# Optimization experiments

Measured on AMD Instinct MI355X. Metric: run time of the kernel, lower is better.

## Reference

```python
import jax, jax.numpy as jnp
import numpy as np

B, S, E, F, N = 2, 1024, 1024, 2048, 8


def setup_inputs() -> dict:
    key = jax.random.key(0)
    k0, k1, k2, k3, k4 = jax.random.split(key, 5)
    x = jax.random.normal(k0, (B, S, E), dtype=jnp.float32)
    # fan_in-scaled params, matching nd_dense_init(1.0, 'fan_in', ...)
    gate_kernel = jax.random.normal(k1, (E, N), dtype=jnp.float32) / np.sqrt(E).astype(np.float32)
    w0 = jax.random.normal(k2, (N, E, F), dtype=jnp.float32) / np.sqrt(E).astype(np.float32)
    w1 = jax.random.normal(k3, (N, E, F), dtype=jnp.float32) / np.sqrt(E).astype(np.float32)
    wo = jax.random.normal(k4, (N, F, E), dtype=jnp.float32) / np.sqrt(F).astype(np.float32)
    return {"x": x, "gate_kernel": gate_kernel, "w0": w0, "w1": w1, "wo": wo, "top_k": 2}


def reference(x, gate_kernel, w0, w1, wo, top_k):
    # x: [B, S, E] -> tokens [T, E]
    b, s, e = x.shape
    n = gate_kernel.shape[-1]
    xf = x.reshape(b * s, e)
    # Router: gate logits + top-k expert selection, softmax over top-k (fp32, as in permute())
    logits = jnp.einsum('te,en->tn', xf, gate_kernel)
    top_w, top_e = jax.lax.top_k(logits, top_k)               # [T, K]
    probs = jax.nn.softmax(top_w.astype(jnp.float32), axis=-1)  # [T, K]
    # Combine weights per (token, expert): scatter top-k probs into [T, N]
    combine = jnp.einsum('tk,tkn->tn', probs, jax.nn.one_hot(top_e, n, dtype=jnp.float32))
    # Expert FFN (dropless): h = silu(x@w0) * (x@w1); out_e = h @ wo   (same math as gmm path)
    h0 = jnp.einsum('te,nef->ntf', xf, w0)                    # [N, T, F]
    h1 = jnp.einsum('te,nef->ntf', xf, w1)
    h = jax.nn.silu(h0) * h1
    expert_out = jnp.einsum('ntf,nfe->nte', h, wo)            # [N, T, E]
    # Weighted combine over experts (matches unpermute's 'BKE,BK->BE' in fp32)
    out = jnp.einsum('nte,tn->te', expert_out, combine)
    return out.reshape(b, s, e)
```

## Files before the change

### kernel.cpp

```cpp
#include <hip/hip_runtime.h>
#include <hip/hip_bf16.h>

#define T_TOK 2048
#define E_DIM 1024
#define F_DIM 2048
#define N_EXP 8

typedef __attribute__((ext_vector_type(8))) short short8;
typedef __attribute__((ext_vector_type(4))) float f32x4;

__device__ __forceinline__ short bf2s(__hip_bfloat16 v) {
  union { __hip_bfloat16 b; short s; } u; u.b = v; return u.s;
}

__device__ __forceinline__ void gload_lds16(const void* g, void* l) {
  __builtin_amdgcn_global_load_lds((const __attribute__((address_space(1))) void*)g,
                                   (__attribute__((address_space(3))) void*)l, 16, 0, 0);
}

__global__ __launch_bounds__(256) void convert_x_kernel(const float* __restrict__ x,
                                                        __hip_bfloat16* __restrict__ xb) {
  size_t i = ((size_t)blockIdx.x * 256 + threadIdx.x) * 8;
  float4 a = *(const float4*)(x + i);
  float4 b = *(const float4*)(x + i + 4);
  short8 o;
  o[0] = bf2s(__float2bfloat16(a.x)); o[1] = bf2s(__float2bfloat16(a.y));
  o[2] = bf2s(__float2bfloat16(a.z)); o[3] = bf2s(__float2bfloat16(a.w));
  o[4] = bf2s(__float2bfloat16(b.x)); o[5] = bf2s(__float2bfloat16(b.y));
  o[6] = bf2s(__float2bfloat16(b.z)); o[7] = bf2s(__float2bfloat16(b.w));
  *(short8*)(xb + i) = o;
}

__global__ __launch_bounds__(256) void transpose_all_kernel(const float* __restrict__ w0,
                                                            const float* __restrict__ w1,
                                                            const float* __restrict__ wo,
                                                            __hip_bfloat16* __restrict__ w0t,
                                                            __hip_bfloat16* __restrict__ w1t,
                                                            __hip_bfloat16* __restrict__ wot) {
  __shared__ float lt[64 * 65];
  int z = blockIdx.z;
  const float* src; __hip_bfloat16* dst;
  int R, C, r0, c0;
  if (z < 16) {
    R = E_DIM; C = F_DIM;
    int e = z & 7;
    src = (z < 8 ? w0 : w1) + (size_t)e * R * C;
    dst = (z < 8 ? w0t : w1t) + (size_t)e * R * C;
    r0 = blockIdx.y * 64; c0 = blockIdx.x * 64;
  } else {
    R = F_DIM; C = E_DIM;
    int e = z - 16;
    src = wo + (size_t)e * R * C;
    dst = wot + (size_t)e * R * C;
    c0 = (blockIdx.x & 15) * 64;
    r0 = (blockIdx.y * 2 + (blockIdx.x >> 4)) * 64;
  }
  int tid = threadIdx.x;
#pragma unroll
  for (int i = 0; i < 4; i++) {
    int chunk = i * 256 + tid;
    int r = chunk >> 4, c4 = (chunk & 15) * 4;
    float4 v = *(const float4*)(src + (size_t)(r0 + r) * C + c0 + c4);
    float* p = &lt[r * 65 + c4];
    p[0] = v.x; p[1] = v.y; p[2] = v.z; p[3] = v.w;
  }
  __syncthreads();
#pragma unroll
  for (int i = 0; i < 2; i++) {
    int chunk = i * 256 + tid;
    int c = chunk >> 3, rr = (chunk & 7) * 8;
    short8 o;
#pragma unroll
    for (int j = 0; j < 8; j++) o[j] = bf2s(__float2bfloat16(lt[(rr + j) * 65 + c]));
    *(short8*)(dst + (size_t)(c0 + c) * R + r0 + rr) = o;
  }
}

__global__ __launch_bounds__(256) void router_kernel(const float* __restrict__ x,
                                                     const float* __restrict__ gk,
                                                     int* __restrict__ tk_e,
                                                     float* __restrict__ tk_p,
                                                     int* __restrict__ counts) {
  int w = threadIdx.x >> 6, l = threadIdx.x & 63;
  int t = blockIdx.x * 4 + w;
  const float* xr = x + (size_t)t * E_DIM;
  double acc[N_EXP];
#pragma unroll
  for (int n = 0; n < N_EXP; n++) acc[n] = 0.0;
  for (int j = 0; j < 16; j++) {
    int i = j * 64 + l;
    double xv = (double)xr[i];
    const float* g = gk + (size_t)i * N_EXP;
#pragma unroll
    for (int n = 0; n < N_EXP; n++) acc[n] += xv * (double)g[n];
  }
#pragma unroll
  for (int off = 32; off > 0; off >>= 1) {
#pragma unroll
    for (int n = 0; n < N_EXP; n++) acc[n] += __shfl_down(acc[n], off);
  }
  if (l == 0) {
    int e1 = 0; double v1 = acc[0];
    for (int n = 1; n < N_EXP; n++) if (acc[n] > v1) { v1 = acc[n]; e1 = n; }
    int e2 = -1; double v2 = -1e300;
    for (int n = 0; n < N_EXP; n++) if (n != e1 && acc[n] > v2) { v2 = acc[n]; e2 = n; }
    float ex = __expf((float)(v2 - v1));
    float p1 = 1.f / (1.f + ex);
    float p2 = ex / (1.f + ex);
    tk_e[t * 2 + 0] = e1; tk_p[t * 2 + 0] = p1;
    tk_e[t * 2 + 1] = e2; tk_p[t * 2 + 1] = p2;
    atomicAdd(&counts[e1], 1);
    atomicAdd(&counts[e2], 1);
  }
}

__global__ __launch_bounds__(256) void scanperm_kernel(const int* __restrict__ tk_e,
                                                       const float* __restrict__ tk_p,
                                                       int* __restrict__ ctrl,
                                                       int* __restrict__ slot_tok,
                                                       float* __restrict__ slot_prob,
                                                       int* __restrict__ inv) {
  __shared__ int offs[8], cur[8];
  int tid = threadIdx.x;
  if (tid == 0) {
    int off = 0, idx = 0;
    for (int e = 0; e < N_EXP; e++) {
      offs[e] = off; cur[e] = 0;
      int c = ctrl[e];
      for (int m0 = 0; m0 < c; m0 += 128) {
        ctrl[32 + idx] = e;
        ctrl[96 + idx] = off + m0;
        ctrl[160 + idx] = (c - m0 < 128) ? (c - m0) : 128;
        idx++;
      }
      off += c;
    }
    ctrl[24] = idx;
  }
  __syncthreads();
  for (int g = tid; g < 2 * T_TOK; g += 256) {
    int e = tk_e[g];
    float p = tk_p[g];
    int pos = atomicAdd(&cur[e], 1);
    int slot = offs[e] + pos;
    slot_tok[slot] = g >> 1;
    slot_prob[slot] = p;
    inv[g] = slot;
  }
}

__global__ __launch_bounds__(512, 4) void gemm1_kernel(const __hip_bfloat16* __restrict__ xb,
                                                       const __hip_bfloat16* __restrict__ w0t,
                                                       const __hip_bfloat16* __restrict__ w1t,
                                                       const int* __restrict__ ctrl,
                                                       const int* __restrict__ slot_tok,
                                                       __hip_bfloat16* __restrict__ h) {
  int lin = blockIdx.x;
  int logical = (lin & 7) * 80 + (lin >> 3);
  int mt = logical % 40;
  int fy = logical / 40;
  if (mt >= ctrl[24]) return;
  int e = ctrl[32 + mt];
  int slot0 = ctrl[96 + mt];
  int rowsv = ctrl[160 + mt];
  int f0 = fy * 128;

  __shared__ alignas(16) short lA[128 * 64];
  __shared__ alignas(16) short lB0[128 * 64];
  __shared__ alignas(16) short lB1[128 * 64];

  int tid = threadIdx.x;
  int w = tid >> 6, l = tid & 63;
  int wm = w >> 2, wn = w & 3;
  int frow = l & 15, fk = l >> 4;

  int r1 = tid >> 3;
  int kc = ((tid & 7) ^ (r1 & 7)) * 8;
  int tokA1 = slot_tok[slot0 + r1];
  int tokA2 = slot_tok[slot0 + r1 + 64];
  const __hip_bfloat16* aS1 = xb + (size_t)tokA1 * E_DIM + kc;
  const __hip_bfloat16* aS2 = xb + (size_t)tokA2 * E_DIM + kc;
  const __hip_bfloat16* b0S1 = w0t + ((size_t)e * F_DIM + f0 + r1) * E_DIM + kc;
  const __hip_bfloat16* b0S2 = b0S1 + (size_t)64 * E_DIM;
  const __hip_bfloat16* b1S1 = w1t + ((size_t)e * F_DIM + f0 + r1) * E_DIM + kc;
  const __hip_bfloat16* b1S2 = b1S1 + (size_t)64 * E_DIM;

  f32x4 zero4 = {0.f, 0.f, 0.f, 0.f};
  f32x4 acc0[4][2], acc1[4][2];
#pragma unroll
  for (int mi = 0; mi < 4; mi++)
#pragma unroll
    for (int ni = 0; ni < 2; ni++) { acc0[mi][ni] = zero4; acc1[mi][ni] = zero4; }

  auto stage = [&](int t) {
    int k0 = t * 64;
    gload_lds16(aS1 + k0,  &lA[w * 512]);
    gload_lds16(aS2 + k0,  &lA[4096 + w * 512]);
    gload_lds16(b0S1 + k0, &lB0[w * 512]);
    gload_lds16(b0S2 + k0, &lB0[4096 + w * 512]);
    gload_lds16(b1S1 + k0, &lB1[w * 512]);
    gload_lds16(b1S2 + k0, &lB1[4096 + w * 512]);
  };

  const int NT = E_DIM / 64;
  for (int t = 0; t < NT; ++t) {
    if (t) __syncthreads();
    stage(t);
    __syncthreads();
    __builtin_amdgcn_s_setprio(1);
#pragma unroll
    for (int ks = 0; ks < 2; ++ks) {
      short8 a[4], b0[2], b1[2];
#pragma unroll
      for (int mi = 0; mi < 4; ++mi) {
        int r = wm * 64 + mi * 16 + frow;
        a[mi] = *(const short8*)&lA[r * 64 + ((ks * 4 + fk) ^ (r & 7)) * 8];
      }
#pragma unroll
      for (int ni = 0; ni < 2; ++ni) {
        int n = wn * 32 + ni * 16 + frow;
        int off = n * 64 + ((ks * 4 + fk) ^ (n & 7)) * 8;
        b0[ni] = *(const short8*)&lB0[off];
        b1[ni] = *(const short8*)&lB1[off];
      }
#pragma unroll
      for (int mi = 0; mi < 4; ++mi)
#pragma unroll
        for (int ni = 0; ni < 2; ++ni) {
          acc0[mi][ni] = __builtin_amdgcn_mfma_f32_16x16x32_bf16(a[mi], b0[ni], acc0[mi][ni], 0, 0, 0);
          acc1[mi][ni] = __builtin_amdgcn_mfma_f32_16x16x32_bf16(a[mi], b1[ni], acc1[mi][ni], 0, 0, 0);
        }
    }
    __builtin_amdgcn_s_setprio(0);
  }

#pragma unroll
  for (int mi = 0; mi < 4; ++mi) {
#pragma unroll
    for (int j = 0; j < 4; ++j) {
      int r = wm * 64 + mi * 16 + fk * 4 + j;
      if (r < rowsv) {
        __hip_bfloat16* hr = h + (size_t)(slot0 + r) * F_DIM + f0 + wn * 32;
#pragma unroll
        for (int ni = 0; ni < 2; ++ni) {
          float v0 = acc0[mi][ni][j];
          float v1 = acc1[mi][ni][j];
          float s = (v0 / (1.f + __expf(-v0))) * v1;
          hr[ni * 16 + frow] = __float2bfloat16(s);
        }
      }
    }
  }
}

__global__ __launch_bounds__(512, 4) void gemm2_kernel(const __hip_bfloat16* __restrict__ h,
                                                       const __hip_bfloat16* __restrict__ wot,
                                                       const int* __restrict__ ctrl,
                                                       const float* __restrict__ slot_prob,
                                                       float* __restrict__ parts) {
  int lin = blockIdx.x;
  int logical = (lin & 7) * 40 + (lin >> 3);
  int mt = logical % 40;
  int ey = logical / 40;
  if (mt >= ctrl[24]) return;
  int e = ctrl[32 + mt];
  int slot0 = ctrl[96 + mt];
  int rowsv = ctrl[160 + mt];
  int e0 = ey * 128;

  __shared__ alignas(16) short lA[128 * 64];
  __shared__ alignas(16) short lB[128 * 64];

  int tid = threadIdx.x;
  int w = tid >> 6, l = tid & 63;
  int wm = w >> 2, wn = w & 3;
  int frow = l & 15, fk = l >> 4;

  int r1 = tid >> 3;
  int kc = ((tid & 7) ^ (r1 & 7)) * 8;
  const __hip_bfloat16* aS1 = h + (size_t)(slot0 + r1) * F_DIM + kc;
  const __hip_bfloat16* aS2 = aS1 + (size_t)64 * F_DIM;
  const __hip_bfloat16* bS1 = wot + ((size_t)e * E_DIM + e0 + r1) * F_DIM + kc;
  const __hip_bfloat16* bS2 = bS1 + (size_t)64 * F_DIM;

  f32x4 zero4 = {0.f, 0.f, 0.f, 0.f};
  f32x4 acc[4][2];
#pragma unroll
  for (int mi = 0; mi < 4; mi++)
#pragma unroll
    for (int ni = 0; ni < 2; ni++) acc[mi][ni] = zero4;

  auto stage = [&](int t) {
    int k0 = t * 64;
    gload_lds16(aS1 + k0, &lA[w * 512]);
    gload_lds16(aS2 + k0, &lA[4096 + w * 512]);
    gload_lds16(bS1 + k0, &lB[w * 512]);
    gload_lds16(bS2 + k0, &lB[4096 + w * 512]);
  };

  const int NT = F_DIM / 64;
  for (int t = 0; t < NT; ++t) {
    if (t) __syncthreads();
    stage(t);
    __syncthreads();
    __builtin_amdgcn_s_setprio(1);
#pragma unroll
    for (int ks = 0; ks < 2; ++ks) {
      short8 a[4], b[2];
#pragma unroll
      for (int mi = 0; mi < 4; ++mi) {
        int r = wm * 64 + mi * 16 + frow;
        a[mi] = *(const short8*)&lA[r * 64 + ((ks * 4 + fk) ^ (r & 7)) * 8];
      }
#pragma unroll
      for (int ni = 0; ni < 2; ++ni) {
        int n = wn * 32 + ni * 16 + frow;
        b[ni] = *(const short8*)&lB[n * 64 + ((ks * 4 + fk) ^ (n & 7)) * 8];
      }
#pragma unroll
      for (int mi = 0; mi < 4; ++mi)
#pragma unroll
        for (int ni = 0; ni < 2; ++ni)
          acc[mi][ni] = __builtin_amdgcn_mfma_f32_16x16x32_bf16(a[mi], b[ni], acc[mi][ni], 0, 0, 0);
    }
    __builtin_amdgcn_s_setprio(0);
  }

#pragma unroll
  for (int mi = 0; mi < 4; ++mi) {
#pragma unroll
    for (int j = 0; j < 4; ++j) {
      int r = wm * 64 + mi * 16 + fk * 4 + j;
      if (r < rowsv) {
        int slot = slot0 + r;
        float p = slot_prob[slot];
        float* pr = parts + (size_t)slot * E_DIM + e0 + wn * 32;
#pragma unroll
        for (int ni = 0; ni < 2; ++ni)
          pr[ni * 16 + frow] = p * acc[mi][ni][j];
      }
    }
  }
}

__global__ __launch_bounds__(256) void combine_kernel(const float* __restrict__ parts,
                                                      const int* __restrict__ inv,
                                                      float* __restrict__ out) {
  int g = blockIdx.x * 256 + threadIdx.x;
  int row = g >> 7, c = (g & 127) * 8;
  int s1 = inv[row * 2], s2 = inv[row * 2 + 1];
  const float4* p1 = (const float4*)(parts + (size_t)s1 * E_DIM + c);
  const float4* p2 = (const float4*)(parts + (size_t)s2 * E_DIM + c);
  float4 a0 = p1[0], a1 = p1[1], b0 = p2[0], b1 = p2[1];
  float4 o0 = {a0.x + b0.x, a0.y + b0.y, a0.z + b0.z, a0.w + b0.w};
  float4 o1 = {a1.x + b1.x, a1.y + b1.y, a1.z + b1.z, a1.w + b1.w};
  float4* op = (float4*)(out + (size_t)row * E_DIM + c);
  op[0] = o0; op[1] = o1;
}

extern "C" void kernel_launch(void* const* d_in, const int* in_sizes, int n_in,
                              void* d_out, int out_size, void* d_ws, size_t ws_size,
                              hipStream_t stream) {
  const float* x  = (const float*)d_in[0];
  const float* gk = (const float*)d_in[1];
  const float* w0 = (const float*)d_in[2];
  const float* w1 = (const float*)d_in[3];
  const float* wo = (const float*)d_in[4];
  float* out = (float*)d_out;
  char* ws = (char*)d_ws;

  const size_t SLOTS = 2 * T_TOK + 128;
  const size_t OFF_XB   = 0;
  const size_t OFF_W0T  = OFF_XB  + (size_t)T_TOK * E_DIM * 2;
  const size_t OFF_W1T  = OFF_W0T + (size_t)N_EXP * E_DIM * F_DIM * 2;
  const size_t OFF_WOT  = OFF_W1T + (size_t)N_EXP * E_DIM * F_DIM * 2;
  const size_t OFF_H    = OFF_WOT + (size_t)N_EXP * F_DIM * E_DIM * 2;
  const size_t OFF_STOK = OFF_H   + SLOTS * F_DIM * 2;
  const size_t OFF_SPRB = OFF_STOK + SLOTS * 4;
  const size_t OFF_TKE  = OFF_SPRB + SLOTS * 4;
  const size_t OFF_TKP  = OFF_TKE + (size_t)2 * T_TOK * 4;
  const size_t OFF_INV  = OFF_TKP + (size_t)2 * T_TOK * 4;
  const size_t OFF_CTRL = OFF_INV + (size_t)2 * T_TOK * 4;
  const size_t NEED     = OFF_CTRL + 1024;
  if (ws_size < NEED) return;

  __hip_bfloat16* xb   = (__hip_bfloat16*)(ws + OFF_XB);
  __hip_bfloat16* w0t  = (__hip_bfloat16*)(ws + OFF_W0T);
  __hip_bfloat16* w1t  = (__hip_bfloat16*)(ws + OFF_W1T);
  __hip_bfloat16* wot  = (__hip_bfloat16*)(ws + OFF_WOT);
  __hip_bfloat16* hbuf = (__hip_bfloat16*)(ws + OFF_H);
  float* parts     = (float*)(ws + OFF_W0T);
  int*   slot_tok  = (int*)(ws + OFF_STOK);
  float* slot_prob = (float*)(ws + OFF_SPRB);
  int*   tk_e      = (int*)(ws + OFF_TKE);
  float* tk_p      = (float*)(ws + OFF_TKP);
  int*   inv       = (int*)(ws + OFF_INV);
  int*   ctrl      = (int*)(ws + OFF_CTRL);

  hipMemsetAsync(ctrl, 0, 1024, stream);
  hipMemsetAsync(slot_tok + 2 * T_TOK, 0, 128 * 4, stream);

  transpose_all_kernel<<<dim3(32, 16, 24), 256, 0, stream>>>(w0, w1, wo, w0t, w1t, wot);
  convert_x_kernel<<<(T_TOK * E_DIM) / (256 * 8), 256, 0, stream>>>(x, xb);
  router_kernel<<<T_TOK / 4, 256, 0, stream>>>(x, gk, tk_e, tk_p, ctrl);
  scanperm_kernel<<<1, 256, 0, stream>>>(tk_e, tk_p, ctrl, slot_tok, slot_prob, inv);
  gemm1_kernel<<<dim3(640), 512, 0, stream>>>(xb, w0t, w1t, ctrl, slot_tok, hbuf);
  gemm2_kernel<<<dim3(320), 512, 0, stream>>>(hbuf, wot, ctrl, slot_prob, parts);
  combine_kernel<<<(T_TOK * 128) / 256, 256, 0, stream>>>(parts, inv, out);
}
```

Baseline: 228.5 us.

## Fuse fp32 weight transpose and bf16 conversion into GEMM B-tile loads

Removes the standalone kernel that transposed and converted all expert weights to bf16. Both GEMM kernels now read fp32 weights directly in their natural layout, convert them to bf16 in registers and write transposed, swizzled short4 chunks into LDS. This avoids a full extra read and write pass over the weights, but every block that shares an expert tile now re-reads fp32 weights (twice the bytes of bf16) and does synchronous register loads instead of async global-to-LDS loads, so load latency is less hidden.

```diff
diff --git a/kernel.cpp b/kernel.cpp
--- a/kernel.cpp
+++ b/kernel.cpp
@@ -8,6 +8,8 @@
 
 typedef __attribute__((ext_vector_type(8))) short short8;
 typedef __attribute__((ext_vector_type(4))) float f32x4;
+
+#define SWZB(f) (((f) ^ ((f) >> 3)) & 7)
 
 __device__ __forceinline__ short bf2s(__hip_bfloat16 v) {
   union { __hip_bfloat16 b; short s; } u; u.b = v; return u.s;
@@ -29,51 +31,6 @@
   o[4] = bf2s(__float2bfloat16(b.x)); o[5] = bf2s(__float2bfloat16(b.y));
   o[6] = bf2s(__float2bfloat16(b.z)); o[7] = bf2s(__float2bfloat16(b.w));
   *(short8*)(xb + i) = o;
-}
-
-__global__ __launch_bounds__(256) void transpose_all_kernel(const float* __restrict__ w0,
-                                                            const float* __restrict__ w1,
-                                                            const float* __restrict__ wo,
-                                                            __hip_bfloat16* __restrict__ w0t,
-                                                            __hip_bfloat16* __restrict__ w1t,
-                                                            __hip_bfloat16* __restrict__ wot) {
-  __shared__ float lt[64 * 65];
-  int z = blockIdx.z;
-  const float* src; __hip_bfloat16* dst;
-  int R, C, r0, c0;
-  if (z < 16) {
-    R = E_DIM; C = F_DIM;
-    int e = z & 7;
-    src = (z < 8 ? w0 : w1) + (size_t)e * R * C;
-    dst = (z < 8 ? w0t : w1t) + (size_t)e * R * C;
-    r0 = blockIdx.y * 64; c0 = blockIdx.x * 64;
-  } else {
-    R = F_DIM; C = E_DIM;
-    int e = z - 16;
-    src = wo + (size_t)e * R * C;
-    dst = wot + (size_t)e * R * C;
-    c0 = (blockIdx.x & 15) * 64;
-    r0 = (blockIdx.y * 2 + (blockIdx.x >> 4)) * 64;
-  }
-  int tid = threadIdx.x;
-#pragma unroll
-  for (int i = 0; i < 4; i++) {
-    int chunk = i * 256 + tid;
-    int r = chunk >> 4, c4 = (chunk & 15) * 4;
-    float4 v = *(const float4*)(src + (size_t)(r0 + r) * C + c0 + c4);
-    float* p = &lt[r * 65 + c4];
-    p[0] = v.x; p[1] = v.y; p[2] = v.z; p[3] = v.w;
-  }
-  __syncthreads();
-#pragma unroll
-  for (int i = 0; i < 2; i++) {
-    int chunk = i * 256 + tid;
-    int c = chunk >> 3, rr = (chunk & 7) * 8;
-    short8 o;
-#pragma unroll
-    for (int j = 0; j < 8; j++) o[j] = bf2s(__float2bfloat16(lt[(rr + j) * 65 + c]));
-    *(short8*)(dst + (size_t)(c0 + c) * R + r0 + rr) = o;
-  }
 }
 
 __global__ __launch_bounds__(256) void router_kernel(const float* __restrict__ x,
@@ -150,8 +107,8 @@
 }
 
 __global__ __launch_bounds__(512, 4) void gemm1_kernel(const __hip_bfloat16* __restrict__ xb,
-                                                       const __hip_bfloat16* __restrict__ w0t,
-                                                       const __hip_bfloat16* __restrict__ w1t,
+                                                       const float* __restrict__ w0,
+                                                       const float* __restrict__ w1,
                                                        const int* __restrict__ ctrl,
                                                        const int* __restrict__ slot_tok,
                                                        __hip_bfloat16* __restrict__ h) {
@@ -175,15 +132,21 @@
   int frow = l & 15, fk = l >> 4;
 
   int r1 = tid >> 3;
-  int kc = ((tid & 7) ^ (r1 & 7)) * 8;
+  int kcA = ((tid & 7) ^ (r1 & 7)) * 8;
   int tokA1 = slot_tok[slot0 + r1];
   int tokA2 = slot_tok[slot0 + r1 + 64];
-  const __hip_bfloat16* aS1 = xb + (size_t)tokA1 * E_DIM + kc;
-  const __hip_bfloat16* aS2 = xb + (size_t)tokA2 * E_DIM + kc;
-  const __hip_bfloat16* b0S1 = w0t + ((size_t)e * F_DIM + f0 + r1) * E_DIM + kc;
-  const __hip_bfloat16* b0S2 = b0S1 + (size_t)64 * E_DIM;
-  const __hip_bfloat16* b1S1 = w1t + ((size_t)e * F_DIM + f0 + r1) * E_DIM + kc;
-  const __hip_bfloat16* b1S2 = b1S1 + (size_t)64 * E_DIM;
+  const __hip_bfloat16* aS1 = xb + (size_t)tokA1 * E_DIM + kcA;
+  const __hip_bfloat16* aS2 = xb + (size_t)tokA2 * E_DIM + kcA;
+
+  int uf = tid & 31, uk = tid >> 5;
+  const float* b0s = w0 + ((size_t)e * E_DIM + uk * 4) * F_DIM + f0 + uf * 4;
+  const float* b1s = w1 + ((size_t)e * E_DIM + uk * 4) * F_DIM + f0 + uf * 4;
+  int elB[4];
+#pragma unroll
+  for (int j = 0; j < 4; ++j) {
+    int f = uf * 4 + j;
+    elB[j] = f * 64 + (((uk >> 1) ^ SWZB(f)) & 7) * 8 + (uk & 1) * 4;
+  }
 
   f32x4 zero4 = {0.f, 0.f, 0.f, 0.f};
   f32x4 acc0[4][2], acc1[4][2];
@@ -191,21 +154,43 @@
   for (int mi = 0; mi < 4; mi++)
 #pragma unroll
     for (int ni = 0; ni < 2; ni++) { acc0[mi][ni] = zero4; acc1[mi][ni] = zero4; }
-
-  auto stage = [&](int t) {
-    int k0 = t * 64;
-    gload_lds16(aS1 + k0,  &lA[w * 512]);
-    gload_lds16(aS2 + k0,  &lA[4096 + w * 512]);
-    gload_lds16(b0S1 + k0, &lB0[w * 512]);
-    gload_lds16(b0S2 + k0, &lB0[4096 + w * 512]);
-    gload_lds16(b1S1 + k0, &lB1[w * 512]);
-    gload_lds16(b1S2 + k0, &lB1[4096 + w * 512]);
-  };
 
   const int NT = E_DIM / 64;
   for (int t = 0; t < NT; ++t) {
     if (t) __syncthreads();
-    stage(t);
+    int k0 = t * 64;
+    gload_lds16(aS1 + k0, &lA[w * 512]);
+    gload_lds16(aS2 + k0, &lA[4096 + w * 512]);
+    {
+      float4 r[4];
+#pragma unroll
+      for (int rr = 0; rr < 4; ++rr)
+        r[rr] = *(const float4*)(b0s + (size_t)(k0 + rr) * F_DIM);
+#pragma unroll
+      for (int j = 0; j < 4; ++j) {
+        short4 q;
+        q.x = bf2s(__float2bfloat16(((const float*)&r[0])[j]));
+        q.y = bf2s(__float2bfloat16(((const float*)&r[1])[j]));
+        q.z = bf2s(__float2bfloat16(((const float*)&r[2])[j]));
+        q.w = bf2s(__float2bfloat16(((const float*)&r[3])[j]));
+        *(short4*)&lB0[elB[j]] = q;
+      }
+    }
+    {
+      float4 r[4];
+#pragma unroll
+      for (int rr = 0; rr < 4; ++rr)
+        r[rr] = *(const float4*)(b1s + (size_t)(k0 + rr) * F_DIM);
+#pragma unroll
+      for (int j = 0; j < 4; ++j) {
+        short4 q;
+        q.x = bf2s(__float2bfloat16(((const float*)&r[0])[j]));
+        q.y = bf2s(__float2bfloat16(((const float*)&r[1])[j]));
+        q.z = bf2s(__float2bfloat16(((const float*)&r[2])[j]));
+        q.w = bf2s(__float2bfloat16(((const float*)&r[3])[j]));
+        *(short4*)&lB1[elB[j]] = q;
+      }
+    }
     __syncthreads();
     __builtin_amdgcn_s_setprio(1);
 #pragma unroll
@@ -219,7 +204,7 @@
 #pragma unroll
       for (int ni = 0; ni < 2; ++ni) {
         int n = wn * 32 + ni * 16 + frow;
-        int off = n * 64 + ((ks * 4 + fk) ^ (n & 7)) * 8;
+        int off = n * 64 + (((ks * 4 + fk) ^ SWZB(n)) & 7) * 8;
         b0[ni] = *(const short8*)&lB0[off];
         b1[ni] = *(const short8*)&lB1[off];
       }
@@ -254,7 +239,7 @@
 }
 
 __global__ __launch_bounds__(512, 4) void gemm2_kernel(const __hip_bfloat16* __restrict__ h,
-                                                       const __hip_bfloat16* __restrict__ wot,
+                                                       const float* __restrict__ wo,
                                                        const int* __restrict__ ctrl,
                                                        const float* __restrict__ slot_prob,
                                                        float* __restrict__ parts) {
@@ -277,11 +262,18 @@
   int frow = l & 15, fk = l >> 4;
 
   int r1 = tid >> 3;
-  int kc = ((tid & 7) ^ (r1 & 7)) * 8;
-  const __hip_bfloat16* aS1 = h + (size_t)(slot0 + r1) * F_DIM + kc;
+  int kcA = ((tid & 7) ^ (r1 & 7)) * 8;
+  const __hip_bfloat16* aS1 = h + (size_t)(slot0 + r1) * F_DIM + kcA;
   const __hip_bfloat16* aS2 = aS1 + (size_t)64 * F_DIM;
-  const __hip_bfloat16* bS1 = wot + ((size_t)e * E_DIM + e0 + r1) * F_DIM + kc;
-  const __hip_bfloat16* bS2 = bS1 + (size_t)64 * F_DIM;
+
+  int ue = tid & 31, uk = tid >> 5;
+  const float* bs = wo + ((size_t)e * F_DIM + uk * 4) * E_DIM + e0 + ue * 4;
+  int elB[4];
+#pragma unroll
+  for (int j = 0; j < 4; ++j) {
+    int f = ue * 4 + j;
+    elB[j] = f * 64 + (((uk >> 1) ^ SWZB(f)) & 7) * 8 + (uk & 1) * 4;
+  }
 
   f32x4 zero4 = {0.f, 0.f, 0.f, 0.f};
   f32x4 acc[4][2];
@@ -290,18 +282,27 @@
 #pragma unroll
     for (int ni = 0; ni < 2; ni++) acc[mi][ni] = zero4;
 
-  auto stage = [&](int t) {
+  const int NT = F_DIM / 64;
+  for (int t = 0; t < NT; ++t) {
+    if (t) __syncthreads();
     int k0 = t * 64;
     gload_lds16(aS1 + k0, &lA[w * 512]);
     gload_lds16(aS2 + k0, &lA[4096 + w * 512]);
-    gload_lds16(bS1 + k0, &lB[w * 512]);
-    gload_lds16(bS2 + k0, &lB[4096 + w * 512]);
-  };
-
-  const int NT = F_DIM / 64;
-  for (int t = 0; t < NT; ++t) {
-    if (t) __syncthreads();
-    stage(t);
+    {
+      float4 r[4];
+#pragma unroll
+      for (int rr = 0; rr < 4; ++rr)
+        r[rr] = *(const float4*)(bs + (size_t)(k0 + rr) * E_DIM);
+#pragma unroll
+      for (int j = 0; j < 4; ++j) {
+        short4 q;
+        q.x = bf2s(__float2bfloat16(((const float*)&r[0])[j]));
+        q.y = bf2s(__float2bfloat16(((const float*)&r[1])[j]));
+        q.z = bf2s(__float2bfloat16(((const float*)&r[2])[j]));
+        q.w = bf2s(__float2bfloat16(((const float*)&r[3])[j]));
+        *(short4*)&lB[elB[j]] = q;
+      }
+    }
     __syncthreads();
     __builtin_amdgcn_s_setprio(1);
 #pragma unroll
@@ -315,7 +316,7 @@
 #pragma unroll
       for (int ni = 0; ni < 2; ++ni) {
         int n = wn * 32 + ni * 16 + frow;
-        b[ni] = *(const short8*)&lB[n * 64 + ((ks * 4 + fk) ^ (n & 7)) * 8];
+        b[ni] = *(const short8*)&lB[n * 64 + (((ks * 4 + fk) ^ SWZB(n)) & 7) * 8];
       }
 #pragma unroll
       for (int mi = 0; mi < 4; ++mi)
@@ -371,11 +372,9 @@
 
   const size_t SLOTS = 2 * T_TOK + 128;
   const size_t OFF_XB   = 0;
-  const size_t OFF_W0T  = OFF_XB  + (size_t)T_TOK * E_DIM * 2;
-  const size_t OFF_W1T  = OFF_W0T + (size_t)N_EXP * E_DIM * F_DIM * 2;
-  const size_t OFF_WOT  = OFF_W1T + (size_t)N_EXP * E_DIM * F_DIM * 2;
-  const size_t OFF_H    = OFF_WOT + (size_t)N_EXP * F_DIM * E_DIM * 2;
-  const size_t OFF_STOK = OFF_H   + SLOTS * F_DIM * 2;
+  const size_t OFF_H    = OFF_XB + (size_t)T_TOK * E_DIM * 2;
+  const size_t OFF_PART = OFF_H + SLOTS * F_DIM * 2;
+  const size_t OFF_STOK = OFF_PART + SLOTS * E_DIM * 4;
   const size_t OFF_SPRB = OFF_STOK + SLOTS * 4;
   const size_t OFF_TKE  = OFF_SPRB + SLOTS * 4;
   const size_t OFF_TKP  = OFF_TKE + (size_t)2 * T_TOK * 4;
@@ -385,11 +384,8 @@
   if (ws_size < NEED) return;
 
   __hip_bfloat16* xb   = (__hip_bfloat16*)(ws + OFF_XB);
-  __hip_bfloat16* w0t  = (__hip_bfloat16*)(ws + OFF_W0T);
-  __hip_bfloat16* w1t  = (__hip_bfloat16*)(ws + OFF_W1T);
-  __hip_bfloat16* wot  = (__hip_bfloat16*)(ws + OFF_WOT);
   __hip_bfloat16* hbuf = (__hip_bfloat16*)(ws + OFF_H);
-  float* parts     = (float*)(ws + OFF_W0T);
+  float* parts     = (float*)(ws + OFF_PART);
   int*   slot_tok  = (int*)(ws + OFF_STOK);
   float* slot_prob = (float*)(ws + OFF_SPRB);
   int*   tk_e      = (int*)(ws + OFF_TKE);
@@ -400,11 +396,10 @@
   hipMemsetAsync(ctrl, 0, 1024, stream);
   hipMemsetAsync(slot_tok + 2 * T_TOK, 0, 128 * 4, stream);
 
-  transpose_all_kernel<<<dim3(32, 16, 24), 256, 0, stream>>>(w0, w1, wo, w0t, w1t, wot);
   convert_x_kernel<<<(T_TOK * E_DIM) / (256 * 8), 256, 0, stream>>>(x, xb);
   router_kernel<<<T_TOK / 4, 256, 0, stream>>>(x, gk, tk_e, tk_p, ctrl);
   scanperm_kernel<<<1, 256, 0, stream>>>(tk_e, tk_p, ctrl, slot_tok, slot_prob, inv);
-  gemm1_kernel<<<dim3(640), 512, 0, stream>>>(xb, w0t, w1t, ctrl, slot_tok, hbuf);
-  gemm2_kernel<<<dim3(320), 512, 0, stream>>>(hbuf, wot, ctrl, slot_prob, parts);
+  gemm1_kernel<<<dim3(640), 512, 0, stream>>>(xb, w0, w1, ctrl, slot_tok, hbuf);
+  gemm2_kernel<<<dim3(320), 512, 0, stream>>>(hbuf, wo, ctrl, slot_prob, parts);
   combine_kernel<<<(T_TOK * 128) / 256, 256, 0, stream>>>(parts, inv, out);
 }
```

After: 221.6 us. -3.0%, faster.

## Double-buffer GEMM LDS tiles with BK=32 and rewrite weight transpose without LDS

Applied to the files above, without the earlier changes.

Both expert GEMM kernels now split LDS into two half-depth (K=32) buffers and prefetch the next tile while MFMAs run on the current one. This cuts the loop from two barriers per iteration to one and lets global-to-LDS loads overlap with compute, using a new XOR swizzle suited to the 32-wide rows. The weight transpose kernel drops shared memory: each thread loads 8 rows of float4 and writes transposed short8 bf16 vectors directly, with out-of-range blocks exiting early. The risks are twice as many loop iterations with smaller MFMA batches per barrier, and less coalesced global stores in the transpose.

```diff
diff --git a/kernel.cpp b/kernel.cpp
--- a/kernel.cpp
+++ b/kernel.cpp
@@ -16,6 +16,10 @@
 __device__ __forceinline__ void gload_lds16(const void* g, void* l) {
   __builtin_amdgcn_global_load_lds((const __attribute__((address_space(1))) void*)g,
                                    (__attribute__((address_space(3))) void*)l, 16, 0, 0);
+}
+
+__device__ __forceinline__ int swz_off(int r, int c8) {
+  return (r >> 1) * 64 + (((((r & 1) << 2) | c8) ^ ((r >> 1) & 7)) * 8);
 }
 
 __global__ __launch_bounds__(256) void convert_x_kernel(const float* __restrict__ x,
@@ -37,42 +41,38 @@
                                                             __hip_bfloat16* __restrict__ w0t,
                                                             __hip_bfloat16* __restrict__ w1t,
                                                             __hip_bfloat16* __restrict__ wot) {
-  __shared__ float lt[64 * 65];
   int z = blockIdx.z;
   const float* src; __hip_bfloat16* dst;
-  int R, C, r0, c0;
+  int R, C;
   if (z < 16) {
     R = E_DIM; C = F_DIM;
+    if (blockIdx.y >= 8) return;
     int e = z & 7;
     src = (z < 8 ? w0 : w1) + (size_t)e * R * C;
     dst = (z < 8 ? w0t : w1t) + (size_t)e * R * C;
-    r0 = blockIdx.y * 64; c0 = blockIdx.x * 64;
   } else {
     R = F_DIM; C = E_DIM;
+    if (blockIdx.x >= 16) return;
     int e = z - 16;
     src = wo + (size_t)e * R * C;
     dst = wot + (size_t)e * R * C;
-    c0 = (blockIdx.x & 15) * 64;
-    r0 = (blockIdx.y * 2 + (blockIdx.x >> 4)) * 64;
-  }
-  int tid = threadIdx.x;
-#pragma unroll
-  for (int i = 0; i < 4; i++) {
-    int chunk = i * 256 + tid;
-    int r = chunk >> 4, c4 = (chunk & 15) * 4;
-    float4 v = *(const float4*)(src + (size_t)(r0 + r) * C + c0 + c4);
-    float* p = &lt[r * 65 + c4];
-    p[0] = v.x; p[1] = v.y; p[2] = v.z; p[3] = v.w;
-  }
-  __syncthreads();
-#pragma unroll
-  for (int i = 0; i < 2; i++) {
-    int chunk = i * 256 + tid;
-    int c = chunk >> 3, rr = (chunk & 7) * 8;
-    short8 o;
-#pragma unroll
-    for (int j = 0; j < 8; j++) o[j] = bf2s(__float2bfloat16(lt[(rr + j) * 65 + c]));
-    *(short8*)(dst + (size_t)(c0 + c) * R + r0 + rr) = o;
+  }
+  int r0 = blockIdx.y * 128, c0 = blockIdx.x * 64;
+  int l = threadIdx.x & 63, w = threadIdx.x >> 6;
+  int r = r0 + 32 * w + 8 * (l >> 4);
+  int c = c0 + 4 * (l & 15);
+
+  float4 v[8];
+#pragma unroll
+  for (int i = 0; i < 8; ++i)
+    v[i] = *(const float4*)(src + (size_t)(r + i) * C + c);
+#pragma unroll
+  for (int j = 0; j < 4; ++j) {
+    short8 q;
+#pragma unroll
+    for (int i = 0; i < 8; ++i)
+      q[i] = bf2s(__float2bfloat16(((const float*)&v[i])[j]));
+    *(short8*)(dst + (size_t)(c + j) * R + r) = q;
   }
 }
 
@@ -165,25 +165,23 @@
   int rowsv = ctrl[160 + mt];
   int f0 = fy * 128;
 
-  __shared__ alignas(16) short lA[128 * 64];
-  __shared__ alignas(16) short lB0[128 * 64];
-  __shared__ alignas(16) short lB1[128 * 64];
+  __shared__ alignas(16) short lA[2][128 * 32];
+  __shared__ alignas(16) short lB0[2][128 * 32];
+  __shared__ alignas(16) short lB1[2][128 * 32];
 
   int tid = threadIdx.x;
   int w = tid >> 6, l = tid & 63;
   int wm = w >> 2, wn = w & 3;
   int frow = l & 15, fk = l >> 4;
 
-  int r1 = tid >> 3;
-  int kc = ((tid & 7) ^ (r1 & 7)) * 8;
-  int tokA1 = slot_tok[slot0 + r1];
-  int tokA2 = slot_tok[slot0 + r1 + 64];
-  const __hip_bfloat16* aS1 = xb + (size_t)tokA1 * E_DIM + kc;
-  const __hip_bfloat16* aS2 = xb + (size_t)tokA2 * E_DIM + kc;
-  const __hip_bfloat16* b0S1 = w0t + ((size_t)e * F_DIM + f0 + r1) * E_DIM + kc;
-  const __hip_bfloat16* b0S2 = b0S1 + (size_t)64 * E_DIM;
-  const __hip_bfloat16* b1S1 = w1t + ((size_t)e * F_DIM + f0 + r1) * E_DIM + kc;
-  const __hip_bfloat16* b1S2 = b1S1 + (size_t)64 * E_DIM;
+  int stripe = tid >> 3, pos = tid & 7;
+  int px = pos ^ (stripe & 7);
+  int sr = (stripe << 1) | (px >> 2);
+  int sc = px & 3;
+  int tokA = slot_tok[slot0 + sr];
+  const __hip_bfloat16* aS  = xb + (size_t)tokA * E_DIM + sc * 8;
+  const __hip_bfloat16* b0S = w0t + ((size_t)e * F_DIM + f0 + sr) * E_DIM + sc * 8;
+  const __hip_bfloat16* b1S = w1t + ((size_t)e * F_DIM + f0 + sr) * E_DIM + sc * 8;
 
   f32x4 zero4 = {0.f, 0.f, 0.f, 0.f};
   f32x4 acc0[4][2], acc1[4][2];
@@ -192,46 +190,43 @@
 #pragma unroll
     for (int ni = 0; ni < 2; ni++) { acc0[mi][ni] = zero4; acc1[mi][ni] = zero4; }
 
-  auto stage = [&](int t) {
-    int k0 = t * 64;
-    gload_lds16(aS1 + k0,  &lA[w * 512]);
-    gload_lds16(aS2 + k0,  &lA[4096 + w * 512]);
-    gload_lds16(b0S1 + k0, &lB0[w * 512]);
-    gload_lds16(b0S2 + k0, &lB0[4096 + w * 512]);
-    gload_lds16(b1S1 + k0, &lB1[w * 512]);
-    gload_lds16(b1S2 + k0, &lB1[4096 + w * 512]);
+  auto stage = [&](int t, int buf) {
+    int k0 = t * 32;
+    gload_lds16(aS + k0,  &lA[buf][w * 512]);
+    gload_lds16(b0S + k0, &lB0[buf][w * 512]);
+    gload_lds16(b1S + k0, &lB1[buf][w * 512]);
   };
 
-  const int NT = E_DIM / 64;
+  stage(0, 0);
+  __syncthreads();
+
+  const int NT = E_DIM / 32;
   for (int t = 0; t < NT; ++t) {
-    if (t) __syncthreads();
-    stage(t);
+    int cur = t & 1;
+    if (t + 1 < NT) stage(t + 1, cur ^ 1);
+    __builtin_amdgcn_s_setprio(1);
+    short8 a[4], b0[2], b1[2];
+#pragma unroll
+    for (int mi = 0; mi < 4; ++mi) {
+      int r = wm * 64 + mi * 16 + frow;
+      a[mi] = *(const short8*)&lA[cur][swz_off(r, fk)];
+    }
+#pragma unroll
+    for (int ni = 0; ni < 2; ++ni) {
+      int n = wn * 32 + ni * 16 + frow;
+      int off = swz_off(n, fk);
+      b0[ni] = *(const short8*)&lB0[cur][off];
+      b1[ni] = *(const short8*)&lB1[cur][off];
+    }
+#pragma unroll
+    for (int mi = 0; mi < 4; ++mi)
+#pragma unroll
+      for (int ni = 0; ni < 2; ++ni) {
+        acc0[mi][ni] = __builtin_amdgcn_mfma_f32_16x16x32_bf16(a[mi], b0[ni], acc0[mi][ni], 0, 0, 0);
+        acc1[mi][ni] = __builtin_amdgcn_mfma_f32_16x16x32_bf16(a[mi], b1[ni], acc1[mi][ni], 0, 0, 0);
+      }
+    __builtin_amdgcn_s_setprio(0);
     __syncthreads();
-    __builtin_amdgcn_s_setprio(1);
-#pragma unroll
-    for (int ks = 0; ks < 2; ++ks) {
-      short8 a[4], b0[2], b1[2];
-#pragma unroll
-      for (int mi = 0; mi < 4; ++mi) {
-        int r = wm * 64 + mi * 16 + frow;
-        a[mi] = *(const short8*)&lA[r * 64 + ((ks * 4 + fk) ^ (r & 7)) * 8];
-      }
-#pragma unroll
-      for (int ni = 0; ni < 2; ++ni) {
-        int n = wn * 32 + ni * 16 + frow;
-        int off = n * 64 + ((ks * 4 + fk) ^ (n & 7)) * 8;
-        b0[ni] = *(const short8*)&lB0[off];
-        b1[ni] = *(const short8*)&lB1[off];
-      }
-#pragma unroll
-      for (int mi = 0; mi < 4; ++mi)
-#pragma unroll
-        for (int ni = 0; ni < 2; ++ni) {
-          acc0[mi][ni] = __builtin_amdgcn_mfma_f32_16x16x32_bf16(a[mi], b0[ni], acc0[mi][ni], 0, 0, 0);
-          acc1[mi][ni] = __builtin_amdgcn_mfma_f32_16x16x32_bf16(a[mi], b1[ni], acc1[mi][ni], 0, 0, 0);
-        }
-    }
-    __builtin_amdgcn_s_setprio(0);
   }
 
 #pragma unroll
@@ -268,20 +263,20 @@
   int rowsv = ctrl[160 + mt];
   int e0 = ey * 128;
 
-  __shared__ alignas(16) short lA[128 * 64];
-  __shared__ alignas(16) short lB[128 * 64];
+  __shared__ alignas(16) short lA[2][128 * 32];
+  __shared__ alignas(16) short lB[2][128 * 32];
 
   int tid = threadIdx.x;
   int w = tid >> 6, l = tid & 63;
   int wm = w >> 2, wn = w & 3;
   int frow = l & 15, fk = l >> 4;
 
-  int r1 = tid >> 3;
-  int kc = ((tid & 7) ^ (r1 & 7)) * 8;
-  const __hip_bfloat16* aS1 = h + (size_t)(slot0 + r1) * F_DIM + kc;
-  const __hip_bfloat16* aS2 = aS1 + (size_t)64 * F_DIM;
-  const __hip_bfloat16* bS1 = wot + ((size_t)e * E_DIM + e0 + r1) * F_DIM + kc;
-  const __hip_bfloat16* bS2 = bS1 + (size_t)64 * F_DIM;
+  int stripe = tid >> 3, pos = tid & 7;
+  int px = pos ^ (stripe & 7);
+  int sr = (stripe << 1) | (px >> 2);
+  int sc = px & 3;
+  const __hip_bfloat16* aS = h + (size_t)(slot0 + sr) * F_DIM + sc * 8;
+  const __hip_bfloat16* bS = wot + ((size_t)e * E_DIM + e0 + sr) * F_DIM + sc * 8;
 
   f32x4 zero4 = {0.f, 0.f, 0.f, 0.f};
   f32x4 acc[4][2];
@@ -290,40 +285,38 @@
 #pragma unroll
     for (int ni = 0; ni < 2; ni++) acc[mi][ni] = zero4;
 
-  auto stage = [&](int t) {
-    int k0 = t * 64;
-    gload_lds16(aS1 + k0, &lA[w * 512]);
-    gload_lds16(aS2 + k0, &lA[4096 + w * 512]);
-    gload_lds16(bS1 + k0, &lB[w * 512]);
-    gload_lds16(bS2 + k0, &lB[4096 + w * 512]);
+  auto stage = [&](int t, int buf) {
+    int k0 = t * 32;
+    gload_lds16(aS + k0, &lA[buf][w * 512]);
+    gload_lds16(bS + k0, &lB[buf][w * 512]);
   };
 
-  const int NT = F_DIM / 64;
+  stage(0, 0);
+  __syncthreads();
+
+  const int NT = F_DIM / 32;
   for (int t = 0; t < NT; ++t) {
-    if (t) __syncthreads();
-    stage(t);
+    int cur = t & 1;
+    if (t + 1 < NT) stage(t + 1, cur ^ 1);
+    __builtin_amdgcn_s_setprio(1);
+    short8 a[4], b[2];
+#pragma unroll
+    for (int mi = 0; mi < 4; ++mi) {
+      int r = wm * 64 + mi * 16 + frow;
+      a[mi] = *(const short8*)&lA[cur][swz_off(r, fk)];
+    }
+#pragma unroll
+    for (int ni = 0; ni < 2; ++ni) {
+      int n = wn * 32 + ni * 16 + frow;
+      b[ni] = *(const short8*)&lB[cur][swz_off(n, fk)];
+    }
+#pragma unroll
+    for (int mi = 0; mi < 4; ++mi)
+#pragma unroll
+      for (int ni = 0; ni < 2; ++ni)
+        acc[mi][ni] = __builtin_amdgcn_mfma_f32_16x16x32_bf16(a[mi], b[ni], acc[mi][ni], 0, 0, 0);
+    __builtin_amdgcn_s_setprio(0);
     __syncthreads();
-    __builtin_amdgcn_s_setprio(1);
-#pragma unroll
-    for (int ks = 0; ks < 2; ++ks) {
-      short8 a[4], b[2];
-#pragma unroll
-      for (int mi = 0; mi < 4; ++mi) {
-        int r = wm * 64 + mi * 16 + frow;
-        a[mi] = *(const short8*)&lA[r * 64 + ((ks * 4 + fk) ^ (r & 7)) * 8];
-      }
-#pragma unroll
-      for (int ni = 0; ni < 2; ++ni) {
-        int n = wn * 32 + ni * 16 + frow;
-        b[ni] = *(const short8*)&lB[n * 64 + ((ks * 4 + fk) ^ (n & 7)) * 8];
-      }
-#pragma unroll
-      for (int mi = 0; mi < 4; ++mi)
-#pragma unroll
-        for (int ni = 0; ni < 2; ++ni)
-          acc[mi][ni] = __builtin_amdgcn_mfma_f32_16x16x32_bf16(a[mi], b[ni], acc[mi][ni], 0, 0, 0);
-    }
-    __builtin_amdgcn_s_setprio(0);
   }
 
 #pragma unroll
```

After: 250.8 us. 9.8% more time.

## Fuse prep kernels and overlap wo transpose with gemm1 blocks

Applied to the files above, without the earlier changes.

Merges the w0/w1 transpose, x conversion and router into a single prep kernel, removing two launches. The wo transpose moves into extra blocks of gemm1, so it can overlap with the first expert GEMM instead of running up front. The transpose tile now converts to bf16 before staging and uses a swizzled short LDS layout, which halves LDS traffic and allows 16-byte stores. The cost is that the extra transpose blocks in gemm1 compete with GEMM blocks for CUs and carry gemm1's LDS allocation.

```diff
diff --git a/kernel.cpp b/kernel.cpp
--- a/kernel.cpp
+++ b/kernel.cpp
@@ -18,71 +18,74 @@
                                    (__attribute__((address_space(3))) void*)l, 16, 0, 0);
 }
 
-__global__ __launch_bounds__(256) void convert_x_kernel(const float* __restrict__ x,
-                                                        __hip_bfloat16* __restrict__ xb) {
-  size_t i = ((size_t)blockIdx.x * 256 + threadIdx.x) * 8;
-  float4 a = *(const float4*)(x + i);
-  float4 b = *(const float4*)(x + i + 4);
-  short8 o;
-  o[0] = bf2s(__float2bfloat16(a.x)); o[1] = bf2s(__float2bfloat16(a.y));
-  o[2] = bf2s(__float2bfloat16(a.z)); o[3] = bf2s(__float2bfloat16(a.w));
-  o[4] = bf2s(__float2bfloat16(b.x)); o[5] = bf2s(__float2bfloat16(b.y));
-  o[6] = bf2s(__float2bfloat16(b.z)); o[7] = bf2s(__float2bfloat16(b.w));
-  *(short8*)(xb + i) = o;
-}
-
-__global__ __launch_bounds__(256) void transpose_all_kernel(const float* __restrict__ w0,
-                                                            const float* __restrict__ w1,
-                                                            const float* __restrict__ wo,
-                                                            __hip_bfloat16* __restrict__ w0t,
-                                                            __hip_bfloat16* __restrict__ w1t,
-                                                            __hip_bfloat16* __restrict__ wot) {
-  __shared__ float lt[64 * 65];
-  int z = blockIdx.z;
-  const float* src; __hip_bfloat16* dst;
-  int R, C, r0, c0;
-  if (z < 16) {
-    R = E_DIM; C = F_DIM;
-    int e = z & 7;
-    src = (z < 8 ? w0 : w1) + (size_t)e * R * C;
-    dst = (z < 8 ? w0t : w1t) + (size_t)e * R * C;
-    r0 = blockIdx.y * 64; c0 = blockIdx.x * 64;
-  } else {
-    R = F_DIM; C = E_DIM;
-    int e = z - 16;
-    src = wo + (size_t)e * R * C;
-    dst = wot + (size_t)e * R * C;
-    c0 = (blockIdx.x & 15) * 64;
-    r0 = (blockIdx.y * 2 + (blockIdx.x >> 4)) * 64;
-  }
-  int tid = threadIdx.x;
-#pragma unroll
-  for (int i = 0; i < 4; i++) {
-    int chunk = i * 256 + tid;
-    int r = chunk >> 4, c4 = (chunk & 15) * 4;
-    float4 v = *(const float4*)(src + (size_t)(r0 + r) * C + c0 + c4);
-    float* p = &lt[r * 65 + c4];
-    p[0] = v.x; p[1] = v.y; p[2] = v.z; p[3] = v.w;
+__device__ __forceinline__ void transpose_tile(const float* __restrict__ src,
+                                               __hip_bfloat16* __restrict__ dst,
+                                               int C, int R, int r0, int c0,
+                                               int tid, short* lds) {
+  int u = tid >> 3, o = tid & 7;
+#pragma unroll
+  for (int it = 0; it < 2; ++it) {
+    int r = it * 32 + u;
+    const float* p = src + (size_t)(r0 + r) * C + c0 + o * 8;
+    float4 v0 = *(const float4*)p;
+    float4 v1 = *(const float4*)(p + 4);
+    float vv[8] = {v0.x, v0.y, v0.z, v0.w, v1.x, v1.y, v1.z, v1.w};
+#pragma unroll
+    for (int j = 0; j < 8; ++j) {
+      int c = o * 8 + j;
+      int rho = (c + (c >> 3)) & 7;
+      lds[c * 64 + ((r + 8 * rho) & 63)] = bf2s(__float2bfloat16(vv[j]));
+    }
   }
   __syncthreads();
 #pragma unroll
-  for (int i = 0; i < 2; i++) {
-    int chunk = i * 256 + tid;
-    int c = chunk >> 3, rr = (chunk & 7) * 8;
-    short8 o;
-#pragma unroll
-    for (int j = 0; j < 8; j++) o[j] = bf2s(__float2bfloat16(lt[(rr + j) * 65 + c]));
-    *(short8*)(dst + (size_t)(c0 + c) * R + r0 + rr) = o;
-  }
-}
-
-__global__ __launch_bounds__(256) void router_kernel(const float* __restrict__ x,
-                                                     const float* __restrict__ gk,
-                                                     int* __restrict__ tk_e,
-                                                     float* __restrict__ tk_p,
-                                                     int* __restrict__ counts) {
+  for (int it = 0; it < 2; ++it) {
+    int c = it * 32 + u;
+    int rho = (c + (c >> 3)) & 7;
+    int b = (o + rho) & 7;
+    short8 q = *(const short8*)&lds[c * 64 + b * 8];
+    *(short8*)(dst + (size_t)(c0 + c) * R + r0 + o * 8) = q;
+  }
+}
+
+__global__ __launch_bounds__(256) void prep_kernel(const float* __restrict__ w0,
+                                                   const float* __restrict__ w1,
+                                                   const float* __restrict__ x,
+                                                   const float* __restrict__ gk,
+                                                   __hip_bfloat16* __restrict__ w0t,
+                                                   __hip_bfloat16* __restrict__ w1t,
+                                                   __hip_bfloat16* __restrict__ xb,
+                                                   int* __restrict__ tk_e,
+                                                   float* __restrict__ tk_p,
+                                                   int* __restrict__ counts) {
+  __shared__ short tl[64 * 64];
+  int bid = blockIdx.x;
+  if (bid < 8192) {
+    int which = bid >> 12;
+    int tile = bid & 4095;
+    int e = tile >> 9;
+    int t2 = tile & 511;
+    int r0 = (t2 & 15) * 64;
+    int c0 = (t2 >> 4) * 64;
+    const float* src = (which ? w1 : w0) + (size_t)e * E_DIM * F_DIM;
+    __hip_bfloat16* dst = (which ? w1t : w0t) + (size_t)e * E_DIM * F_DIM;
+    transpose_tile(src, dst, F_DIM, E_DIM, r0, c0, threadIdx.x, tl);
+    return;
+  }
+  if (bid < 8192 + 1024) {
+    size_t i = ((size_t)(bid - 8192) * 256 + threadIdx.x) * 8;
+    float4 a = *(const float4*)(x + i);
+    float4 b = *(const float4*)(x + i + 4);
+    short8 oo;
+    oo[0] = bf2s(__float2bfloat16(a.x)); oo[1] = bf2s(__float2bfloat16(a.y));
+    oo[2] = bf2s(__float2bfloat16(a.z)); oo[3] = bf2s(__float2bfloat16(a.w));
+    oo[4] = bf2s(__float2bfloat16(b.x)); oo[5] = bf2s(__float2bfloat16(b.y));
+    oo[6] = bf2s(__float2bfloat16(b.z)); oo[7] = bf2s(__float2bfloat16(b.w));
+    *(short8*)(xb + i) = oo;
+    return;
+  }
   int w = threadIdx.x >> 6, l = threadIdx.x & 63;
-  int t = blockIdx.x * 4 + w;
+  int t = (bid - 9216) * 4 + w;
   const float* xr = x + (size_t)t * E_DIM;
   double acc[N_EXP];
 #pragma unroll
@@ -154,7 +157,26 @@
                                                        const __hip_bfloat16* __restrict__ w1t,
                                                        const int* __restrict__ ctrl,
                                                        const int* __restrict__ slot_tok,
-                                                       __hip_bfloat16* __restrict__ h) {
+                                                       __hip_bfloat16* __restrict__ h,
+                                                       const float* __restrict__ wo,
+                                                       __hip_bfloat16* __restrict__ wot) {
+  __shared__ alignas(16) short lA[128 * 64];
+  __shared__ alignas(16) short lB0[128 * 64];
+  __shared__ alignas(16) short lB1[128 * 64];
+
+  if (blockIdx.x >= 640) {
+    int half = threadIdx.x >> 8, tt = threadIdx.x & 255;
+    int tile = (blockIdx.x - 640) * 2 + half;
+    int e = tile >> 9;
+    int t2 = tile & 511;
+    int r0 = (t2 & 31) * 64;
+    int c0 = (t2 >> 5) * 64;
+    short* tl = half ? (short*)lB0 : (short*)lA;
+    transpose_tile(wo + (size_t)e * F_DIM * E_DIM, wot + (size_t)e * E_DIM * F_DIM,
+                   E_DIM, F_DIM, r0, c0, tt, tl);
+    return;
+  }
+
   int lin = blockIdx.x;
   int logical = (lin & 7) * 80 + (lin >> 3);
   int mt = logical % 40;
@@ -164,10 +186,6 @@
   int slot0 = ctrl[96 + mt];
   int rowsv = ctrl[160 + mt];
   int f0 = fy * 128;
-
-  __shared__ alignas(16) short lA[128 * 64];
-  __shared__ alignas(16) short lB0[128 * 64];
-  __shared__ alignas(16) short lB1[128 * 64];
 
   int tid = threadIdx.x;
   int w = tid >> 6, l = tid & 63;
@@ -400,11 +418,9 @@
   hipMemsetAsync(ctrl, 0, 1024, stream);
   hipMemsetAsync(slot_tok + 2 * T_TOK, 0, 128 * 4, stream);
 
-  transpose_all_kernel<<<dim3(32, 16, 24), 256, 0, stream>>>(w0, w1, wo, w0t, w1t, wot);
-  convert_x_kernel<<<(T_TOK * E_DIM) / (256 * 8), 256, 0, stream>>>(x, xb);
-  router_kernel<<<T_TOK / 4, 256, 0, stream>>>(x, gk, tk_e, tk_p, ctrl);
+  prep_kernel<<<9728, 256, 0, stream>>>(w0, w1, x, gk, w0t, w1t, xb, tk_e, tk_p, ctrl);
   scanperm_kernel<<<1, 256, 0, stream>>>(tk_e, tk_p, ctrl, slot_tok, slot_prob, inv);
-  gemm1_kernel<<<dim3(640), 512, 0, stream>>>(xb, w0t, w1t, ctrl, slot_tok, hbuf);
-  gemm2_kernel<<<dim3(320), 512, 0, stream>>>(hbuf, wot, ctrl, slot_prob, parts);
+  gemm1_kernel<<<2688, 512, 0, stream>>>(xb, w0t, w1t, ctrl, slot_tok, hbuf, wo, wot);
+  gemm2_kernel<<<320, 512, 0, stream>>>(hbuf, wot, ctrl, slot_prob, parts);
   combine_kernel<<<(T_TOK * 128) / 256, 256, 0, stream>>>(parts, inv, out);
 }
```

New measurement: 217.8 us. -4.7%, faster.
